# Optimization experiments

Measured on AMD Instinct MI355X. Metric: run time of the kernel, lower is better.

The kernel has to match this reference:

```python
import jax, jax.numpy as jnp
import numpy as np

NUM_CLASSES = 2
THRESH = 0.5        # overlap_thresh
NEGPOS = 3          # neg:pos ratio
VAR = (0.1, 0.2)    # cfg['variance']
B, P, O = 64, 32768, 50


def point_form(p):
    # center-size [cx,cy,w,h] -> corner [xmin,ymin,xmax,ymax]
    return jnp.concatenate([p[:, :2] - p[:, 2:] * 0.5, p[:, :2] + p[:, 2:] * 0.5], axis=1)


def iou(a, b):
    # a [O,4], b [P,4] corner form -> [O,P]
    lt = jnp.maximum(a[:, None, :2], b[None, :, :2])
    rb = jnp.minimum(a[:, None, 2:], b[None, :, 2:])
    wh = jnp.clip(rb - lt, 0.0, None)
    inter = wh[..., 0] * wh[..., 1]
    area_a = ((a[:, 2] - a[:, 0]) * (a[:, 3] - a[:, 1]))[:, None]
    area_b = ((b[:, 2] - b[:, 0]) * (b[:, 3] - b[:, 1]))[None, :]
    return inter / (area_a + area_b - inter)


def encode(matched, priors_cs):
    g_cxcy = ((matched[:, :2] + matched[:, 2:]) * 0.5 - priors_cs[:, :2]) / (VAR[0] * priors_cs[:, 2:])
    g_wh = jnp.log((matched[:, 2:] - matched[:, :2]) / priors_cs[:, 2:]) / VAR[1]
    return jnp.concatenate([g_cxcy, g_wh], axis=1)


def match_one(truths, labels, priors_cs, priors_pt):
    ovl = iou(truths, priors_pt)                # [O,P]
    best_prior_idx = jnp.argmax(ovl, axis=1)    # [O] best prior per GT
    best_truth_ovl = jnp.max(ovl, axis=0)       # [P]
    best_truth_idx = jnp.argmax(ovl, axis=0)    # [P]
    best_truth_ovl = best_truth_ovl.at[best_prior_idx].set(2.0)
    best_truth_idx = best_truth_idx.at[best_prior_idx].set(jnp.arange(truths.shape[0]))
    matched = truths[best_truth_idx]            # [P,4]
    conf = jnp.where(best_truth_ovl < THRESH, 0, labels[best_truth_idx])
    return encode(matched, priors_cs), conf


def reference(arm_loc, arm_conf, odm_loc, odm_conf, priors, targets):
    loc_data, conf_data = arm_loc, arm_conf    # use_ARM=False -> ARM branch
    num, num_priors = loc_data.shape[0], loc_data.shape[1]
    truths = targets[..., :4]
    labels = (targets[..., 4] >= 0).astype(jnp.int32)   # num_classes == 2 binarization
    priors_pt = point_form(priors)
    loc_t, conf_t = jax.vmap(lambda t, l: match_one(t, l, priors, priors_pt))(truths, labels)
    loc_t = jax.lax.stop_gradient(loc_t)
    conf_t = jax.lax.stop_gradient(conf_t)
    pos = conf_t > 0                             # [B,P]
    # localization: smooth L1, summed over positives
    d = loc_data - loc_t
    ad = jnp.abs(d)
    sl1 = jnp.where(ad < 1.0, 0.5 * d * d, ad - 0.5)
    loss_l = jnp.sum(sl1 * pos[..., None].astype(loc_data.dtype))
    # per-prior conf loss for hard negative mining
    lse = jax.nn.logsumexp(conf_data, axis=-1)   # [B,P]
    picked = jnp.take_along_axis(conf_data, conf_t[..., None], axis=-1)[..., 0]
    lc = lse - picked                            # NLL per prior
    lc_mine = jnp.where(pos, 0.0, lc)            # zero positives before ranking
    order = jnp.argsort(-lc_mine, axis=1)        # descending sort
    rank = jnp.argsort(order, axis=1)            # rank of each prior
    num_pos = jnp.sum(pos, axis=1, keepdims=True)            # [B,1]
    num_neg = jnp.minimum(NEGPOS * num_pos, num_priors - 1)
    neg = rank < num_neg
    sel = (pos | neg).astype(conf_data.dtype)
    loss_c = jnp.sum(lc * sel)
    N = jnp.sum(num_pos).astype(loc_data.dtype)
    return loss_l / N, loss_c / N


def setup_inputs():
    key = jax.random.key(0)
    ks = jax.random.split(key, 8)
    arm_loc = jax.random.normal(ks[0], (B, P, 4), jnp.float32)
    arm_conf = jax.random.normal(ks[1], (B, P, NUM_CLASSES), jnp.float32)
    odm_loc = jax.random.normal(ks[2], (B, P, 4), jnp.float32)
    odm_conf = jax.random.normal(ks[3], (B, P, NUM_CLASSES), jnp.float32)
    # priors in center-size form
    p_cxcy = jax.random.uniform(ks[4], (P, 2), jnp.float32, 0.05, 0.95)
    p_wh = jax.random.uniform(ks[5], (P, 2), jnp.float32, 0.05, 0.5)
    priors = jnp.concatenate([p_cxcy, p_wh], axis=1)
    # GT boxes in corner form with valid extents, labels >= 0
    t_cxcy = jax.random.uniform(ks[6], (B, O, 2), jnp.float32, 0.2, 0.8)
    t_wh = jax.random.uniform(ks[7], (B, O, 2), jnp.float32, 0.05, 0.3)
    boxes = jnp.concatenate([t_cxcy - t_wh * 0.5, t_cxcy + t_wh * 0.5], axis=-1)
    targets = jnp.concatenate([boxes, jnp.ones((B, O, 1), jnp.float32)], axis=-1)
    return {"arm_loc": arm_loc, "arm_conf": arm_conf, "odm_loc": odm_loc,
            "odm_conf": odm_conf, "priors": priors, "targets": targets}
```

## Files before the change

kernel.cpp:

```cpp
#include <hip/hip_runtime.h>
#include <cstdint>

#pragma clang fp contract(off)

#define BB 64
#define PP 32768
#define OO 50
#define THRESH_F 0.5f
#define VAR0 0.1f
#define VAR1 0.2f
#define NEGPOS_I 3
#define SS 32
#define T1 4
#define NB0 2048
#define NB12 1024

typedef unsigned long long u64;

__global__ void k_zero(float4* __restrict__ dst, int n4) {
    int i = blockIdx.x * blockDim.x + threadIdx.x;
    if (i < n4) dst[i] = make_float4(0.f, 0.f, 0.f, 0.f);
}

#define DPP_MAX(x, ctrl, rmask)                                              \
    x = fmaxf(x, __int_as_float(__builtin_amdgcn_update_dpp(                 \
            0, __float_as_int(x), (ctrl), (rmask), 0xf, true)));

__global__ void __launch_bounds__(256, 8)
k_match(const float* __restrict__ priors, const float* __restrict__ targets,
        float* __restrict__ bto, int* __restrict__ bti, u64* __restrict__ bpm) {
    __shared__ float tr4[OO * 4];
    __shared__ float trA[OO];
    int b = blockIdx.y, tid = threadIdx.x;
    for (int i = tid; i < OO * 4; i += 256)
        tr4[i] = targets[(size_t)(b * OO + (i >> 2)) * 5 + (i & 3)];
    __syncthreads();
    if (tid < OO)
        trA[tid] = (tr4[tid*4+2] - tr4[tid*4]) * (tr4[tid*4+3] - tr4[tid*4+1]);
    __syncthreads();

    int p0 = blockIdx.x * (256 * T1) + tid * T1;
    float bx0[T1], by0[T1], bx1[T1], by1[T1], aB[T1];
#pragma unroll
    for (int j = 0; j < T1; ++j) {
        float4 pr = ((const float4*)priors)[p0 + j];
        bx0[j] = pr.x - pr.z * 0.5f; by0[j] = pr.y - pr.w * 0.5f;
        bx1[j] = pr.x + pr.z * 0.5f; by1[j] = pr.y + pr.w * 0.5f;
        aB[j] = (bx1[j] - bx0[j]) * (by1[j] - by0[j]);
    }
    float rbv[T1]; int rbi[T1];
#pragma unroll
    for (int j = 0; j < T1; ++j) { rbv[j] = -1.0f; rbi[j] = 0; }

    for (int t = 0; t < OO; ++t) {
        float t0 = tr4[t*4], t1v = tr4[t*4+1], t2 = tr4[t*4+2], t3 = tr4[t*4+3];
        float aA = trA[t];
        float cbv = -1.0f; int cbp = 0;
#pragma unroll
        for (int j = 0; j < T1; ++j) {
            float ltx = fmaxf(t0, bx0[j]), lty = fmaxf(t1v, by0[j]);
            float rbx = fminf(t2, bx1[j]), rby = fminf(t3, by1[j]);
            float wx = fmaxf(rbx - ltx, 0.f), wy = fmaxf(rby - lty, 0.f);
            float inter = wx * wy;
            float v = inter / (aA + aB[j] - inter);
            if (v > rbv[j]) { rbv[j] = v; rbi[j] = t; }
            if (v > cbv) { cbv = v; cbp = p0 + j; }
        }
        float x = cbv;
        DPP_MAX(x, 0x111, 0xf);
        DPP_MAX(x, 0x112, 0xf);
        DPP_MAX(x, 0x114, 0xf);
        DPP_MAX(x, 0x118, 0xf);
        DPP_MAX(x, 0x142, 0xa);
        DPP_MAX(x, 0x143, 0xc);
        float mv = __int_as_float(__builtin_amdgcn_readlane(__float_as_int(x), 63));
        unsigned long long msk = __ballot(cbv == mv);
        int lane = (int)__ffsll((long long)msk) - 1;
        int pwin = __builtin_amdgcn_readlane(cbp, lane);
        if ((tid & 63) == 0) {
            u64 pk = ((u64)__float_as_uint(mv) << 32) | (unsigned)(PP - pwin);
            atomicMax(&bpm[b * OO + t], pk);
        }
    }
    size_t bp = (size_t)b * PP + p0;
    ((float4*)bto)[bp >> 2] = make_float4(rbv[0], rbv[1], rbv[2], rbv[3]);
    ((int4*)bti)[bp >> 2]   = make_int4(rbi[0], rbi[1], rbi[2], rbi[3]);
}

__global__ void k_force(const u64* __restrict__ bpm,
                        float* __restrict__ bto, int* __restrict__ bti) {
    __shared__ int pidx[OO];
    int b = blockIdx.x, tid = threadIdx.x;
    if (tid < OO) pidx[tid] = PP - (int)(unsigned)(bpm[b * OO + tid] & 0xFFFFFFFFull);
    __syncthreads();
    if (tid == 0) {
        for (int j = 0; j < OO; ++j) {
            int p = pidx[j];
            bto[(size_t)b * PP + p] = 2.0f;
            bti[(size_t)b * PP + p] = j;
        }
    }
}

__global__ void __launch_bounds__(256)
k_loss(const float* __restrict__ arm_loc, const float* __restrict__ arm_conf,
       const float* __restrict__ priors, const float* __restrict__ targets,
       const float* __restrict__ bto, const int* __restrict__ bti,
       float* __restrict__ lcm, float* __restrict__ pll,
       float* __restrict__ pplc, int* __restrict__ pnp) {
    int b = blockIdx.y, s = blockIdx.x, tid = threadIdx.x;
    int p = s * 1024 + tid * 4;
    size_t bp = (size_t)b * PP + p;

    float4 ov4 = ((const float4*)bto)[bp >> 2];
    int4   ti4 = ((const int4*)bti)[bp >> 2];
    float4 ca  = ((const float4*)arm_conf)[bp >> 1];
    float4 cb  = ((const float4*)arm_conf)[(bp >> 1) + 1];
    float ovs[4] = {ov4.x, ov4.y, ov4.z, ov4.w};
    int   tis[4] = {ti4.x, ti4.y, ti4.z, ti4.w};
    float cs[8]  = {ca.x, ca.y, ca.z, ca.w, cb.x, cb.y, cb.z, cb.w};

    float ll = 0.0f, plc = 0.0f; int np = 0;
    float outv[4];
    for (int c = 0; c < 4; ++c) {
        int ti = tis[c];
        const float* tb = &targets[(size_t)(b * OO + ti) * 5];
        int label = (tb[4] >= 0.0f) ? 1 : 0;
        int conf = (ovs[c] < THRESH_F) ? 0 : label;
        float c0 = cs[c * 2], c1 = cs[c * 2 + 1];
        float m = fmaxf(c0, c1);
        float lse = logf(expf(c0 - m) + expf(c1 - m)) + m;
        float picked = (conf == 1) ? c1 : c0;
        float lc = lse - picked;
        bool pos = conf > 0;
        outv[c] = pos ? 0.0f : lc;
        if (pos) {
            np++; plc += lc;
            float4 pr = ((const float4*)priors)[p + c];
            float gx = ((tb[0] + tb[2]) * 0.5f - pr.x) / (VAR0 * pr.z);
            float gy = ((tb[1] + tb[3]) * 0.5f - pr.y) / (VAR0 * pr.w);
            float gw = logf((tb[2] - tb[0]) / pr.z) / VAR1;
            float gh = logf((tb[3] - tb[1]) / pr.w) / VAR1;
            float g[4] = {gx, gy, gw, gh};
            float4 ld = ((const float4*)arm_loc)[bp + c];
            float lds_[4] = {ld.x, ld.y, ld.z, ld.w};
            for (int q = 0; q < 4; ++q) {
                float d = lds_[q] - g[q];
                float ad = fabsf(d);
                ll += (ad < 1.0f) ? 0.5f * d * d : ad - 0.5f;
            }
        }
    }
    ((float4*)lcm)[bp >> 2] = make_float4(outv[0], outv[1], outv[2], outv[3]);

    __shared__ float s1[256], s2[256]; __shared__ int s3[256];
    s1[tid] = ll; s2[tid] = plc; s3[tid] = np;
    __syncthreads();
    for (int st = 128; st > 0; st >>= 1) {
        if (tid < st) { s1[tid] += s1[tid+st]; s2[tid] += s2[tid+st]; s3[tid] += s3[tid+st]; }
        __syncthreads();
    }
    if (tid == 0) {
        pll[s * BB + b] = s1[0];
        pplc[s * BB + b] = s2[0];
        pnp[s * BB + b] = s3[0];
    }
}

template <int PASS>
__global__ void __launch_bounds__(256)
k_hist(const float* __restrict__ lcm, const unsigned* __restrict__ spre,
       int* __restrict__ Hc, float* __restrict__ Hs) {
    const int nbins = (PASS == 0) ? NB0 : NB12;
    __shared__ int hc[NB0]; __shared__ float hs[NB0];
    int b = blockIdx.y, tid = threadIdx.x;
    for (int i = tid; i < nbins; i += 256) { hc[i] = 0; hs[i] = 0.f; }
    __syncthreads();
    unsigned pref = (PASS == 0) ? 0u : spre[b];
    const float4* v4 = (const float4*)(lcm + (size_t)b * PP);
    int base = blockIdx.x * 1024;
    for (int i = 0; i < 4; ++i) {
        float4 x = v4[base + i * 256 + tid];
        float xs[4] = {x.x, x.y, x.z, x.w};
        for (int c = 0; c < 4; ++c) {
            unsigned u = __float_as_uint(xs[c]);
            bool ok; unsigned bin;
            if (PASS == 0)      { ok = true;               bin = u >> 20; }
            else if (PASS == 1) { ok = (u >> 20) == pref;  bin = (u >> 10) & 1023u; }
            else                { ok = (u >> 10) == pref;  bin = u & 1023u; }
            if (ok) { atomicAdd(&hc[bin], 1); atomicAdd(&hs[bin], xs[c]); }
        }
    }
    __syncthreads();
    for (int i = tid; i < nbins; i += 256) {
        int cv = hc[i];
        if (cv) {
            atomicAdd(&Hc[b * nbins + i], cv);
            atomicAdd(&Hs[b * nbins + i], hs[i]);
        }
    }
}

__global__ void __launch_bounds__(256)
k_scan(const int* __restrict__ Hc, const float* __restrict__ Hs, int nbins,
       int pass, const int* __restrict__ pnp, unsigned* __restrict__ spre,
       int* __restrict__ srem, float* __restrict__ ssum,
       unsigned* __restrict__ stb) {
    int b = blockIdx.x, tid = threadIdx.x;
    int CH = nbins >> 8;
    const int* hc = Hc + b * nbins;
    const float* hs = Hs + b * nbins;
    __shared__ int sc[256]; __shared__ float sf[256];
    __shared__ int s_chunk; __shared__ int s_r; __shared__ float s_S;

    int c = 0; float f = 0.f;
    int base = tid * CH;
    for (int i = 0; i < CH; ++i) { c += hc[base + i]; f += hs[base + i]; }
    sc[tid] = c; sf[tid] = f;
    __syncthreads();
    for (int off = 1; off < 256; off <<= 1) {
        int cv = (tid + off < 256) ? sc[tid + off] : 0;
        float fv = (tid + off < 256) ? sf[tid + off] : 0.f;
        __syncthreads();
        sc[tid] += cv; sf[tid] += fv;
        __syncthreads();
    }
    if (tid == 0) {
        int r; float S;
        if (pass == 0) {
            int np = 0;
            for (int i = 0; i < SS; ++i) np += pnp[i * BB + b];
            int k = NEGPOS_I * np; if (k > PP - 1) k = PP - 1;
            r = k; S = 0.f;
        } else { r = srem[b]; S = ssum[b]; }
        s_r = r; s_S = S;
    }
    __syncthreads();
    int r = s_r;
    int nxt = (tid == 255) ? 0 : sc[tid + 1];
    if (sc[tid] >= r && nxt < r) s_chunk = tid;
    __syncthreads();
    if (tid == 0) {
        int ch = s_chunk;
        int r2 = r - ((ch == 255) ? 0 : sc[ch + 1]);
        float S2 = s_S + ((ch == 255) ? 0.f : sf[ch + 1]);
        int binSel = ch * CH;
        for (int i = CH - 1; i >= 0; --i) {
            int bin = ch * CH + i;
            int cb = hc[bin];
            if (r2 <= cb) { binSel = bin; break; }
            r2 -= cb; S2 += hs[bin];
        }
        unsigned pref = (pass == 0) ? (unsigned)binSel
                                    : ((spre[b] << 10) | (unsigned)binSel);
        spre[b] = pref; srem[b] = r2; ssum[b] = S2;
        if (pass == 2) stb[b] = pref;
    }
}

__global__ void k_final(const float* __restrict__ pll, const float* __restrict__ pplc,
                        const int* __restrict__ pnp, const float* __restrict__ ssum,
                        const int* __restrict__ srem, const unsigned* __restrict__ stb,
                        float* __restrict__ out) {
    int b = threadIdx.x;
    float ll = 0.f, plc = 0.f; int np = 0;
    for (int s = 0; s < SS; ++s) {
        ll += pll[s * BB + b];
        plc += pplc[s * BB + b];
        np += pnp[s * BB + b];
    }
    float tval = __uint_as_float(stb[b]);
    float cc = plc + ssum[b] + (float)srem[b] * tval;
    for (int s = 32; s > 0; s >>= 1) {
        ll += __shfl_down(ll, s);
        cc += __shfl_down(cc, s);
        np += __shfl_down(np, s);
    }
    if (b == 0) {
        float N = (float)np;
        out[0] = ll / N;
        out[1] = cc / N;
    }
}

extern "C" void kernel_launch(void* const* d_in, const int* in_sizes, int n_in,
                              void* d_out, int out_size, void* d_ws, size_t ws_size,
                              hipStream_t stream) {
    const float* arm_loc  = (const float*)d_in[0];
    const float* arm_conf = (const float*)d_in[1];
    const float* priors   = (const float*)d_in[4];
    const float* targets  = (const float*)d_in[5];
    float* out = (float*)d_out;

    char* w = (char*)d_ws;
    float* bto = (float*)w;  w += sizeof(float) * (size_t)BB * PP;
    int*   bti = (int*)w;    w += sizeof(int)   * (size_t)BB * PP;
    float* lcm = (float*)w;  w += sizeof(float) * (size_t)BB * PP;
    char* zbase = w;
    int*   Hc0 = (int*)w;    w += sizeof(int)   * BB * NB0;
    float* Hs0 = (float*)w;  w += sizeof(float) * BB * NB0;
    int*   Hc1 = (int*)w;    w += sizeof(int)   * BB * NB12;
    float* Hs1 = (float*)w;  w += sizeof(float) * BB * NB12;
    int*   Hc2 = (int*)w;    w += sizeof(int)   * BB * NB12;
    float* Hs2 = (float*)w;  w += sizeof(float) * BB * NB12;
    u64*   bpm = (u64*)w;    w += sizeof(u64)   * BB * OO;
    size_t zbytes = (size_t)(w - zbase);
    float* pll  = (float*)w; w += sizeof(float) * BB * SS;
    float* pplc = (float*)w; w += sizeof(float) * BB * SS;
    int*   pnp  = (int*)w;   w += sizeof(int)   * BB * SS;
    unsigned* spre = (unsigned*)w; w += sizeof(unsigned) * BB;
    int*      srem = (int*)w;      w += sizeof(int) * BB;
    float*    ssum = (float*)w;    w += sizeof(float) * BB;
    unsigned* stb  = (unsigned*)w; w += sizeof(unsigned) * BB;

    int n4 = (int)(zbytes / 16);
    k_zero<<<(n4 + 255) / 256, 256, 0, stream>>>((float4*)zbase, n4);
    k_match<<<dim3(PP / (256 * T1), BB), 256, 0, stream>>>(priors, targets, bto, bti, bpm);
    k_force<<<BB, 64, 0, stream>>>(bpm, bto, bti);
    k_loss<<<dim3(SS, BB), 256, 0, stream>>>(arm_loc, arm_conf, priors, targets,
                                             bto, bti, lcm, pll, pplc, pnp);
    k_hist<0><<<dim3(8, BB), 256, 0, stream>>>(lcm, spre, Hc0, Hs0);
    k_scan<<<BB, 256, 0, stream>>>(Hc0, Hs0, NB0, 0, pnp, spre, srem, ssum, stb);
    k_hist<1><<<dim3(8, BB), 256, 0, stream>>>(lcm, spre, Hc1, Hs1);
    k_scan<<<BB, 256, 0, stream>>>(Hc1, Hs1, NB12, 1, pnp, spre, srem, ssum, stb);
    k_hist<2><<<dim3(8, BB), 256, 0, stream>>>(lcm, spre, Hc2, Hs2);
    k_scan<<<BB, 256, 0, stream>>>(Hc2, Hs2, NB12, 2, pnp, spre, srem, ssum, stb);
    k_final<<<1, 64, 0, stream>>>(pll, pplc, pnp, ssum, srem, stb, out);
}
```

Baseline: 283.4 us.

## Fuse matching, loss and first histogram pass; patch forced matches afterward

Merges the matching kernel with the per-prior loss computation and the first radix histogram pass, so the overlap and index arrays no longer go to global memory and come back. A packed byte per prior records positivity and matched truth index. A small fix-up kernel then applies the forced best-prior matches as deltas to the loss sums and the histogram. The two remaining histogram and scan passes are folded into one kernel per batch row, which cuts the launch count. In exchange, each selection block scans its whole row twice, and the delta approach relies on the packed index fitting in 6 bits and on deduplicating forced priors correctly.

```diff
diff --git a/kernel.cpp b/kernel.cpp
--- a/kernel.cpp
+++ b/kernel.cpp
@@ -23,17 +23,47 @@
 }
 
 #define DPP_MAX(x, ctrl, rmask)                                              \
-    x = fmaxf(x, __int_as_float(__builtin_amdgcn_update_dpp(                 \
-            0, __float_as_int(x), (ctrl), (rmask), 0xf, true)));
+    {                                                                        \
+        int _o = __float_as_int(x);                                          \
+        x = fmaxf(x, __int_as_float(__builtin_amdgcn_update_dpp(             \
+                _o, _o, (ctrl), (rmask), 0xf, false)));                      \
+    }
+
+__device__ __forceinline__ float sl1enc(const float* __restrict__ tb,
+                                        float4 pr, float4 ld) {
+    float gx = ((tb[0] + tb[2]) * 0.5f - pr.x) / (VAR0 * pr.z);
+    float gy = ((tb[1] + tb[3]) * 0.5f - pr.y) / (VAR0 * pr.w);
+    float gw = logf((tb[2] - tb[0]) / pr.z) / VAR1;
+    float gh = logf((tb[3] - tb[1]) / pr.w) / VAR1;
+    float g[4] = {gx, gy, gw, gh};
+    float l[4] = {ld.x, ld.y, ld.z, ld.w};
+    float s = 0.f;
+    for (int q = 0; q < 4; ++q) {
+        float d = l[q] - g[q];
+        float ad = fabsf(d);
+        s += (ad < 1.0f) ? 0.5f * d * d : ad - 0.5f;
+    }
+    return s;
+}
 
 __global__ void __launch_bounds__(256, 8)
-k_match(const float* __restrict__ priors, const float* __restrict__ targets,
-        float* __restrict__ bto, int* __restrict__ bti, u64* __restrict__ bpm) {
+k_ml(const float* __restrict__ priors, const float* __restrict__ targets,
+     const float* __restrict__ arm_loc, const float* __restrict__ arm_conf,
+     float* __restrict__ lcm, unsigned char* __restrict__ bpi,
+     u64* __restrict__ bpm,
+     float* __restrict__ pll, float* __restrict__ pplc, int* __restrict__ pnp,
+     int* __restrict__ Hc0, float* __restrict__ Hs0) {
     __shared__ float tr4[OO * 4];
     __shared__ float trA[OO];
+    __shared__ int   trL[OO];
+    __shared__ int   hc[NB0];
+    __shared__ float hs[NB0];
     int b = blockIdx.y, tid = threadIdx.x;
     for (int i = tid; i < OO * 4; i += 256)
         tr4[i] = targets[(size_t)(b * OO + (i >> 2)) * 5 + (i & 3)];
+    if (tid < OO)
+        trL[tid] = (targets[(size_t)(b * OO + tid) * 5 + 4] >= 0.0f) ? 1 : 0;
+    for (int i = tid; i < NB0; i += 256) { hc[i] = 0; hs[i] = 0.f; }
     __syncthreads();
     if (tid < OO)
         trA[tid] = (tr4[tid*4+2] - tr4[tid*4]) * (tr4[tid*4+3] - tr4[tid*4+1]);
@@ -82,78 +112,50 @@
             atomicMax(&bpm[b * OO + t], pk);
         }
     }
+
     size_t bp = (size_t)b * PP + p0;
-    ((float4*)bto)[bp >> 2] = make_float4(rbv[0], rbv[1], rbv[2], rbv[3]);
-    ((int4*)bti)[bp >> 2]   = make_int4(rbi[0], rbi[1], rbi[2], rbi[3]);
-}
-
-__global__ void k_force(const u64* __restrict__ bpm,
-                        float* __restrict__ bto, int* __restrict__ bti) {
-    __shared__ int pidx[OO];
-    int b = blockIdx.x, tid = threadIdx.x;
-    if (tid < OO) pidx[tid] = PP - (int)(unsigned)(bpm[b * OO + tid] & 0xFFFFFFFFull);
-    __syncthreads();
-    if (tid == 0) {
-        for (int j = 0; j < OO; ++j) {
-            int p = pidx[j];
-            bto[(size_t)b * PP + p] = 2.0f;
-            bti[(size_t)b * PP + p] = j;
-        }
-    }
-}
-
-__global__ void __launch_bounds__(256)
-k_loss(const float* __restrict__ arm_loc, const float* __restrict__ arm_conf,
-       const float* __restrict__ priors, const float* __restrict__ targets,
-       const float* __restrict__ bto, const int* __restrict__ bti,
-       float* __restrict__ lcm, float* __restrict__ pll,
-       float* __restrict__ pplc, int* __restrict__ pnp) {
-    int b = blockIdx.y, s = blockIdx.x, tid = threadIdx.x;
-    int p = s * 1024 + tid * 4;
-    size_t bp = (size_t)b * PP + p;
-
-    float4 ov4 = ((const float4*)bto)[bp >> 2];
-    int4   ti4 = ((const int4*)bti)[bp >> 2];
-    float4 ca  = ((const float4*)arm_conf)[bp >> 1];
-    float4 cb  = ((const float4*)arm_conf)[(bp >> 1) + 1];
-    float ovs[4] = {ov4.x, ov4.y, ov4.z, ov4.w};
-    int   tis[4] = {ti4.x, ti4.y, ti4.z, ti4.w};
-    float cs[8]  = {ca.x, ca.y, ca.z, ca.w, cb.x, cb.y, cb.z, cb.w};
+    float4 ca = ((const float4*)arm_conf)[bp >> 1];
+    float4 cb = ((const float4*)arm_conf)[(bp >> 1) + 1];
+    float cs[8] = {ca.x, ca.y, ca.z, ca.w, cb.x, cb.y, cb.z, cb.w};
 
     float ll = 0.0f, plc = 0.0f; int np = 0;
-    float outv[4];
+    float outv[4]; unsigned pbyte = 0;
+#pragma unroll
     for (int c = 0; c < 4; ++c) {
-        int ti = tis[c];
-        const float* tb = &targets[(size_t)(b * OO + ti) * 5];
-        int label = (tb[4] >= 0.0f) ? 1 : 0;
-        int conf = (ovs[c] < THRESH_F) ? 0 : label;
-        float c0 = cs[c * 2], c1 = cs[c * 2 + 1];
+        int ti = rbi[c]; float ov = rbv[c];
+        int conf = (ov < THRESH_F) ? 0 : trL[ti];
+        float c0 = cs[c*2], c1 = cs[c*2+1];
         float m = fmaxf(c0, c1);
         float lse = logf(expf(c0 - m) + expf(c1 - m)) + m;
-        float picked = (conf == 1) ? c1 : c0;
-        float lc = lse - picked;
         bool pos = conf > 0;
+        float lc = lse - (pos ? c1 : c0);
         outv[c] = pos ? 0.0f : lc;
+        pbyte |= (unsigned)((pos ? 0x80u : 0u) | (unsigned)ti) << (8 * c);
+        unsigned u = __float_as_uint(outv[c]);
+        atomicAdd(&hc[u >> 20], 1);
+        atomicAdd(&hs[u >> 20], outv[c]);
         if (pos) {
             np++; plc += lc;
-            float4 pr = ((const float4*)priors)[p + c];
-            float gx = ((tb[0] + tb[2]) * 0.5f - pr.x) / (VAR0 * pr.z);
-            float gy = ((tb[1] + tb[3]) * 0.5f - pr.y) / (VAR0 * pr.w);
-            float gw = logf((tb[2] - tb[0]) / pr.z) / VAR1;
-            float gh = logf((tb[3] - tb[1]) / pr.w) / VAR1;
-            float g[4] = {gx, gy, gw, gh};
+            float4 pr = ((const float4*)priors)[p0 + c];
             float4 ld = ((const float4*)arm_loc)[bp + c];
-            float lds_[4] = {ld.x, ld.y, ld.z, ld.w};
-            for (int q = 0; q < 4; ++q) {
-                float d = lds_[q] - g[q];
-                float ad = fabsf(d);
-                ll += (ad < 1.0f) ? 0.5f * d * d : ad - 0.5f;
-            }
+            ll += sl1enc(&tr4[ti * 4], pr, ld);
         }
     }
     ((float4*)lcm)[bp >> 2] = make_float4(outv[0], outv[1], outv[2], outv[3]);
-
-    __shared__ float s1[256], s2[256]; __shared__ int s3[256];
+    ((unsigned*)bpi)[bp >> 2] = pbyte;
+
+    __syncthreads();
+    for (int i = tid; i < NB0; i += 256) {
+        int cv = hc[i];
+        if (cv) {
+            atomicAdd(&Hc0[b * NB0 + i], cv);
+            atomicAdd(&Hs0[b * NB0 + i], hs[i]);
+        }
+    }
+    __syncthreads();
+    float* s1 = (float*)hc;
+    int*   s3 = hc + 256;
+    float* s2 = hs;
     s1[tid] = ll; s2[tid] = plc; s3[tid] = np;
     __syncthreads();
     for (int st = 128; st > 0; st >>= 1) {
@@ -161,100 +163,202 @@
         __syncthreads();
     }
     if (tid == 0) {
-        pll[s * BB + b] = s1[0];
-        pplc[s * BB + b] = s2[0];
-        pnp[s * BB + b] = s3[0];
-    }
-}
-
-template <int PASS>
+        pll[blockIdx.x * BB + b] = s1[0];
+        pplc[blockIdx.x * BB + b] = s2[0];
+        pnp[blockIdx.x * BB + b] = s3[0];
+    }
+}
+
+__global__ void k_fix(const u64* __restrict__ bpm, const float* __restrict__ targets,
+                      const float* __restrict__ arm_loc, const float* __restrict__ arm_conf,
+                      const float* __restrict__ priors, const unsigned char* __restrict__ bpi,
+                      float* __restrict__ lcm,
+                      float* __restrict__ pll, float* __restrict__ pplc,
+                      int* __restrict__ pnp, int* __restrict__ npb,
+                      int* __restrict__ Hc0, float* __restrict__ Hs0) {
+    int b = blockIdx.x, j = threadIdx.x;
+    int p = -1;
+    if (j < OO) p = PP - (int)(unsigned)(bpm[b * OO + j] & 0xFFFFFFFFull);
+    bool w = (j < OO);
+    for (int jj = 1; jj < OO; ++jj) {
+        int pj = __shfl(p, jj, 64);
+        if (jj > j && pj == p) w = false;
+    }
+    float dll = 0.f, dplc = 0.f; int dnp = 0;
+    if (w) {
+        size_t bp = (size_t)b * PP + p;
+        unsigned char ob = bpi[bp];
+        bool old_pos = (ob & 0x80u) != 0;
+        int old_ti = ob & 63;
+        float2 cf = ((const float2*)arm_conf)[bp];
+        float c0 = cf.x, c1 = cf.y;
+        float m = fmaxf(c0, c1);
+        float lse = logf(expf(c0 - m) + expf(c1 - m)) + m;
+        const float* tbj = &targets[(size_t)(b * OO + j) * 5];
+        bool new_pos = (tbj[4] >= 0.0f);
+        float old_lcm = lcm[bp];
+        float new_lcm = new_pos ? 0.0f : (lse - c0);
+        unsigned uo = __float_as_uint(old_lcm), un = __float_as_uint(new_lcm);
+        if (uo != un) {
+            atomicAdd(&Hc0[b * NB0 + (uo >> 20)], -1);
+            atomicAdd(&Hs0[b * NB0 + (uo >> 20)], -old_lcm);
+            atomicAdd(&Hc0[b * NB0 + (un >> 20)], 1);
+            atomicAdd(&Hs0[b * NB0 + (un >> 20)], new_lcm);
+            lcm[bp] = new_lcm;
+        }
+        float4 pr = ((const float4*)priors)[p];
+        float4 ld = ((const float4*)arm_loc)[bp];
+        if (old_pos) {
+            dnp -= 1; dplc -= (lse - c1);
+            dll -= sl1enc(&targets[(size_t)(b * OO + old_ti) * 5], pr, ld);
+        }
+        if (new_pos) {
+            dnp += 1; dplc += (lse - c1);
+            dll += sl1enc(tbj, pr, ld);
+        }
+    }
+    int myp = (j < SS) ? pnp[j * BB + b] : 0;
+    for (int s = 32; s >= 1; s >>= 1) {
+        dll += __shfl_down(dll, s, 64);
+        dplc += __shfl_down(dplc, s, 64);
+        dnp += __shfl_down(dnp, s, 64);
+        myp += __shfl_down(myp, s, 64);
+    }
+    if (j == 0) {
+        pll[b] += dll;
+        pplc[b] += dplc;
+        pnp[b] += dnp;
+        npb[b] = myp + dnp;
+    }
+}
+
 __global__ void __launch_bounds__(256)
-k_hist(const float* __restrict__ lcm, const unsigned* __restrict__ spre,
-       int* __restrict__ Hc, float* __restrict__ Hs) {
-    const int nbins = (PASS == 0) ? NB0 : NB12;
-    __shared__ int hc[NB0]; __shared__ float hs[NB0];
-    int b = blockIdx.y, tid = threadIdx.x;
-    for (int i = tid; i < nbins; i += 256) { hc[i] = 0; hs[i] = 0.f; }
-    __syncthreads();
-    unsigned pref = (PASS == 0) ? 0u : spre[b];
-    const float4* v4 = (const float4*)(lcm + (size_t)b * PP);
-    int base = blockIdx.x * 1024;
-    for (int i = 0; i < 4; ++i) {
-        float4 x = v4[base + i * 256 + tid];
-        float xs[4] = {x.x, x.y, x.z, x.w};
-        for (int c = 0; c < 4; ++c) {
-            unsigned u = __float_as_uint(xs[c]);
-            bool ok; unsigned bin;
-            if (PASS == 0)      { ok = true;               bin = u >> 20; }
-            else if (PASS == 1) { ok = (u >> 20) == pref;  bin = (u >> 10) & 1023u; }
-            else                { ok = (u >> 10) == pref;  bin = u & 1023u; }
-            if (ok) { atomicAdd(&hc[bin], 1); atomicAdd(&hs[bin], xs[c]); }
-        }
-    }
-    __syncthreads();
-    for (int i = tid; i < nbins; i += 256) {
-        int cv = hc[i];
-        if (cv) {
-            atomicAdd(&Hc[b * nbins + i], cv);
-            atomicAdd(&Hs[b * nbins + i], hs[i]);
-        }
-    }
-}
-
-__global__ void __launch_bounds__(256)
-k_scan(const int* __restrict__ Hc, const float* __restrict__ Hs, int nbins,
-       int pass, const int* __restrict__ pnp, unsigned* __restrict__ spre,
-       int* __restrict__ srem, float* __restrict__ ssum,
-       unsigned* __restrict__ stb) {
+k_sel(const float* __restrict__ lcm, const int* __restrict__ npb,
+      int* __restrict__ Hc0, float* __restrict__ Hs0,
+      float* __restrict__ ssum, int* __restrict__ srem, unsigned* __restrict__ stb) {
+    __shared__ int hc[NB12]; __shared__ float hs[NB12];
+    __shared__ int sc[256]; __shared__ float sf[256];
+    __shared__ int s_chunk, s_r; __shared__ float s_S; __shared__ unsigned s_pref;
     int b = blockIdx.x, tid = threadIdx.x;
-    int CH = nbins >> 8;
-    const int* hc = Hc + b * nbins;
-    const float* hs = Hs + b * nbins;
-    __shared__ int sc[256]; __shared__ float sf[256];
-    __shared__ int s_chunk; __shared__ int s_r; __shared__ float s_S;
-
-    int c = 0; float f = 0.f;
-    int base = tid * CH;
-    for (int i = 0; i < CH; ++i) { c += hc[base + i]; f += hs[base + i]; }
-    sc[tid] = c; sf[tid] = f;
-    __syncthreads();
-    for (int off = 1; off < 256; off <<= 1) {
-        int cv = (tid + off < 256) ? sc[tid + off] : 0;
-        float fv = (tid + off < 256) ? sf[tid + off] : 0.f;
-        __syncthreads();
-        sc[tid] += cv; sf[tid] += fv;
-        __syncthreads();
-    }
-    if (tid == 0) {
-        int r; float S;
-        if (pass == 0) {
-            int np = 0;
-            for (int i = 0; i < SS; ++i) np += pnp[i * BB + b];
-            int k = NEGPOS_I * np; if (k > PP - 1) k = PP - 1;
-            r = k; S = 0.f;
-        } else { r = srem[b]; S = ssum[b]; }
-        s_r = r; s_S = S;
-    }
-    __syncthreads();
-    int r = s_r;
-    int nxt = (tid == 255) ? 0 : sc[tid + 1];
-    if (sc[tid] >= r && nxt < r) s_chunk = tid;
-    __syncthreads();
-    if (tid == 0) {
-        int ch = s_chunk;
-        int r2 = r - ((ch == 255) ? 0 : sc[ch + 1]);
-        float S2 = s_S + ((ch == 255) ? 0.f : sf[ch + 1]);
-        int binSel = ch * CH;
-        for (int i = CH - 1; i >= 0; --i) {
-            int bin = ch * CH + i;
-            int cb = hc[bin];
-            if (r2 <= cb) { binSel = bin; break; }
-            r2 -= cb; S2 += hs[bin];
-        }
-        unsigned pref = (pass == 0) ? (unsigned)binSel
-                                    : ((spre[b] << 10) | (unsigned)binSel);
-        spre[b] = pref; srem[b] = r2; ssum[b] = S2;
-        if (pass == 2) stb[b] = pref;
+
+    {
+        const int* hcg = Hc0 + b * NB0; const float* hsg = Hs0 + b * NB0;
+        int c = 0; float f = 0.f; int base = tid * 8;
+        for (int i = 0; i < 8; ++i) { c += hcg[base + i]; f += hsg[base + i]; }
+        sc[tid] = c; sf[tid] = f;
+        if (tid == 0) {
+            int k = NEGPOS_I * npb[b]; if (k > PP - 1) k = PP - 1;
+            s_r = k; s_S = 0.f;
+        }
+        __syncthreads();
+        for (int off = 1; off < 256; off <<= 1) {
+            int cv = (tid + off < 256) ? sc[tid + off] : 0;
+            float fv = (tid + off < 256) ? sf[tid + off] : 0.f;
+            __syncthreads(); sc[tid] += cv; sf[tid] += fv; __syncthreads();
+        }
+        int r = s_r;
+        int nxt = (tid == 255) ? 0 : sc[tid + 1];
+        if (sc[tid] >= r && nxt < r) s_chunk = tid;
+        __syncthreads();
+        if (tid == 0) {
+            int ch = s_chunk;
+            int r2 = r - ((ch == 255) ? 0 : sc[ch + 1]);
+            float S2 = s_S + ((ch == 255) ? 0.f : sf[ch + 1]);
+            int binSel = ch * 8;
+            for (int i = 7; i >= 0; --i) {
+                int bin = ch * 8 + i; int cbn = hcg[bin];
+                if (r2 <= cbn) { binSel = bin; break; }
+                r2 -= cbn; S2 += hsg[bin];
+            }
+            s_pref = (unsigned)binSel; s_r = r2; s_S = S2;
+        }
+        __syncthreads();
+    }
+    {
+        for (int i = tid; i < NB12; i += 256) { hc[i] = 0; hs[i] = 0.f; }
+        __syncthreads();
+        unsigned pref = s_pref;
+        const float4* v4 = (const float4*)(lcm + (size_t)b * PP);
+        for (int it = 0; it < 32; ++it) {
+            float4 x = v4[it * 256 + tid];
+            float xs[4] = {x.x, x.y, x.z, x.w};
+            for (int c2 = 0; c2 < 4; ++c2) {
+                unsigned u = __float_as_uint(xs[c2]);
+                if ((u >> 20) == pref) {
+                    atomicAdd(&hc[(u >> 10) & 1023u], 1);
+                    atomicAdd(&hs[(u >> 10) & 1023u], xs[c2]);
+                }
+            }
+        }
+        __syncthreads();
+        int c = 0; float f = 0.f; int base = tid * 4;
+        for (int i = 0; i < 4; ++i) { c += hc[base + i]; f += hs[base + i]; }
+        sc[tid] = c; sf[tid] = f; __syncthreads();
+        for (int off = 1; off < 256; off <<= 1) {
+            int cv = (tid + off < 256) ? sc[tid + off] : 0;
+            float fv = (tid + off < 256) ? sf[tid + off] : 0.f;
+            __syncthreads(); sc[tid] += cv; sf[tid] += fv; __syncthreads();
+        }
+        int r = s_r;
+        int nxt = (tid == 255) ? 0 : sc[tid + 1];
+        if (sc[tid] >= r && nxt < r) s_chunk = tid;
+        __syncthreads();
+        if (tid == 0) {
+            int ch = s_chunk;
+            int r2 = r - ((ch == 255) ? 0 : sc[ch + 1]);
+            float S2 = s_S + ((ch == 255) ? 0.f : sf[ch + 1]);
+            int binSel = ch * 4;
+            for (int i = 3; i >= 0; --i) {
+                int bin = ch * 4 + i; int cbn = hc[bin];
+                if (r2 <= cbn) { binSel = bin; break; }
+                r2 -= cbn; S2 += hs[bin];
+            }
+            s_pref = (s_pref << 10) | (unsigned)binSel; s_r = r2; s_S = S2;
+        }
+        __syncthreads();
+    }
+    {
+        for (int i = tid; i < NB12; i += 256) { hc[i] = 0; hs[i] = 0.f; }
+        __syncthreads();
+        unsigned pref = s_pref;
+        const float4* v4 = (const float4*)(lcm + (size_t)b * PP);
+        for (int it = 0; it < 32; ++it) {
+            float4 x = v4[it * 256 + tid];
+            float xs[4] = {x.x, x.y, x.z, x.w};
+            for (int c2 = 0; c2 < 4; ++c2) {
+                unsigned u = __float_as_uint(xs[c2]);
+                if ((u >> 10) == pref) {
+                    atomicAdd(&hc[u & 1023u], 1);
+                    atomicAdd(&hs[u & 1023u], xs[c2]);
+                }
+            }
+        }
+        __syncthreads();
+        int c = 0; float f = 0.f; int base = tid * 4;
+        for (int i = 0; i < 4; ++i) { c += hc[base + i]; f += hs[base + i]; }
+        sc[tid] = c; sf[tid] = f; __syncthreads();
+        for (int off = 1; off < 256; off <<= 1) {
+            int cv = (tid + off < 256) ? sc[tid + off] : 0;
+            float fv = (tid + off < 256) ? sf[tid + off] : 0.f;
+            __syncthreads(); sc[tid] += cv; sf[tid] += fv; __syncthreads();
+        }
+        int r = s_r;
+        int nxt = (tid == 255) ? 0 : sc[tid + 1];
+        if (sc[tid] >= r && nxt < r) s_chunk = tid;
+        __syncthreads();
+        if (tid == 0) {
+            int ch = s_chunk;
+            int r2 = r - ((ch == 255) ? 0 : sc[ch + 1]);
+            float S2 = s_S + ((ch == 255) ? 0.f : sf[ch + 1]);
+            int binSel = ch * 4;
+            for (int i = 3; i >= 0; --i) {
+                int bin = ch * 4 + i; int cbn = hc[bin];
+                if (r2 <= cbn) { binSel = bin; break; }
+                r2 -= cbn; S2 += hs[bin];
+            }
+            stb[b] = (s_pref << 10) | (unsigned)binSel;
+            srem[b] = r2; ssum[b] = S2;
+        }
     }
 }
 
@@ -293,37 +397,28 @@
     float* out = (float*)d_out;
 
     char* w = (char*)d_ws;
-    float* bto = (float*)w;  w += sizeof(float) * (size_t)BB * PP;
-    int*   bti = (int*)w;    w += sizeof(int)   * (size_t)BB * PP;
     float* lcm = (float*)w;  w += sizeof(float) * (size_t)BB * PP;
+    unsigned char* bpi = (unsigned char*)w; w += (size_t)BB * PP;
     char* zbase = w;
     int*   Hc0 = (int*)w;    w += sizeof(int)   * BB * NB0;
     float* Hs0 = (float*)w;  w += sizeof(float) * BB * NB0;
-    int*   Hc1 = (int*)w;    w += sizeof(int)   * BB * NB12;
-    float* Hs1 = (float*)w;  w += sizeof(float) * BB * NB12;
-    int*   Hc2 = (int*)w;    w += sizeof(int)   * BB * NB12;
-    float* Hs2 = (float*)w;  w += sizeof(float) * BB * NB12;
     u64*   bpm = (u64*)w;    w += sizeof(u64)   * BB * OO;
     size_t zbytes = (size_t)(w - zbase);
     float* pll  = (float*)w; w += sizeof(float) * BB * SS;
     float* pplc = (float*)w; w += sizeof(float) * BB * SS;
     int*   pnp  = (int*)w;   w += sizeof(int)   * BB * SS;
-    unsigned* spre = (unsigned*)w; w += sizeof(unsigned) * BB;
+    int*   npb  = (int*)w;   w += sizeof(int)   * BB;
+    unsigned* spre_unused = (unsigned*)w; w += sizeof(unsigned) * BB; (void)spre_unused;
     int*      srem = (int*)w;      w += sizeof(int) * BB;
     float*    ssum = (float*)w;    w += sizeof(float) * BB;
     unsigned* stb  = (unsigned*)w; w += sizeof(unsigned) * BB;
 
     int n4 = (int)(zbytes / 16);
     k_zero<<<(n4 + 255) / 256, 256, 0, stream>>>((float4*)zbase, n4);
-    k_match<<<dim3(PP / (256 * T1), BB), 256, 0, stream>>>(priors, targets, bto, bti, bpm);
-    k_force<<<BB, 64, 0, stream>>>(bpm, bto, bti);
-    k_loss<<<dim3(SS, BB), 256, 0, stream>>>(arm_loc, arm_conf, priors, targets,
-                                             bto, bti, lcm, pll, pplc, pnp);
-    k_hist<0><<<dim3(8, BB), 256, 0, stream>>>(lcm, spre, Hc0, Hs0);
-    k_scan<<<BB, 256, 0, stream>>>(Hc0, Hs0, NB0, 0, pnp, spre, srem, ssum, stb);
-    k_hist<1><<<dim3(8, BB), 256, 0, stream>>>(lcm, spre, Hc1, Hs1);
-    k_scan<<<BB, 256, 0, stream>>>(Hc1, Hs1, NB12, 1, pnp, spre, srem, ssum, stb);
-    k_hist<2><<<dim3(8, BB), 256, 0, stream>>>(lcm, spre, Hc2, Hs2);
-    k_scan<<<BB, 256, 0, stream>>>(Hc2, Hs2, NB12, 2, pnp, spre, srem, ssum, stb);
+    k_ml<<<dim3(SS, BB), 256, 0, stream>>>(priors, targets, arm_loc, arm_conf,
+                                           lcm, bpi, bpm, pll, pplc, pnp, Hc0, Hs0);
+    k_fix<<<BB, 64, 0, stream>>>(bpm, targets, arm_loc, arm_conf, priors, bpi,
+                                 lcm, pll, pplc, pnp, npb, Hc0, Hs0);
+    k_sel<<<BB, 256, 0, stream>>>(lcm, npb, Hc0, Hs0, ssum, srem, stb);
     k_final<<<1, 64, 0, stream>>>(pll, pplc, pnp, ssum, srem, stb, out);
 }
```

New measurement: 267.1 us. 1.06x faster.
